# Kernel optimization log

Measured on AMD Instinct MI355X. Metric: run time of the kernel, lower is better.

## Reference

```python
import jax, jax.numpy as jnp
import numpy as np

INPUT_DIM = 1024
OUTPUT_DIM = 1024


def setup_inputs() -> dict:
    key = jax.random.key(0)
    k1, k2, k3, k4 = jax.random.split(key, 4)
    B, S, D = 4, 2048, INPUT_DIM
    src = jax.random.normal(k1, (B, S, D), dtype=jnp.float32)
    tgt = jax.random.normal(k2, (B, S, D), dtype=jnp.float32)
    # nn.Linear(input_dim*2, output_dim): weight [out, in], bias [out]
    bound = 1.0 / np.sqrt(2 * D)
    W = jax.random.uniform(k3, (OUTPUT_DIM, 2 * D), jnp.float32, -bound, bound)
    b = jax.random.uniform(k4, (OUTPUT_DIM,), jnp.float32, -bound, bound)
    return {"src": src, "tgt": tgt, "W": W, "b": b}


def reference(src, tgt, W, b):
    # weight = bmm(tgt, src^T): [B, S_tgt, S_src]
    weight = jnp.einsum("btd,bsd->bts", tgt, src)
    # NOTE: original uses Softmax(dim=1) -> normalizes over the tgt axis
    weight = jax.nn.softmax(weight, axis=1)
    # weighted sum over src positions: [B, S_tgt, D]
    weight_sum = jnp.einsum("bts,bsd->btd", weight, src)
    output = jnp.concatenate([weight_sum, tgt], axis=2)  # [B, S_tgt, 2D]
    output = output @ W.T + b  # [B, S_tgt, output_dim]
    return (output, weight)
```

## Files before the change

### kernel.cpp

```cpp
#include <hip/hip_runtime.h>
#include <stdint.h>


#define B_   4
#define S_   2048
#define D_   1024
#define OUTD 1024

typedef unsigned short ushort_t;
typedef _Float16 half8 __attribute__((ext_vector_type(8)));
typedef float    f32x4 __attribute__((ext_vector_type(4)));

__device__ __forceinline__ ushort_t f2h(float f) {
    union { _Float16 h; ushort_t u; } v;
    v.h = (_Float16)f;
    return v.u;
}
__device__ __forceinline__ float h2f(ushort_t u) {
    union { _Float16 h; ushort_t u; } v;
    v.u = u;
    return (float)v.h;
}

__device__ __forceinline__ void ld16(const ushort_t* g, ushort_t* l) {
    __builtin_amdgcn_global_load_lds(
        (const __attribute__((address_space(1))) void*)g,
        (__attribute__((address_space(3))) void*)l, 16, 0, 0);
}


__global__ void k_split(const float4* __restrict__ src, const float4* __restrict__ tgt,
                        ushort4* __restrict__ sh,
                        ushort4* __restrict__ th, ushort4* __restrict__ tl)
{
    const int64_t n4 = (int64_t)B_ * S_ * D_ / 4;
    for (int64_t i = (int64_t)blockIdx.x * blockDim.x + threadIdx.x; i < n4;
         i += (int64_t)gridDim.x * blockDim.x) {
        float4 s = src[i];
        sh[i] = (ushort4){f2h(s.x), f2h(s.y), f2h(s.z), f2h(s.w)};
        float4 tv = tgt[i];
        ushort4 ht = {f2h(tv.x), f2h(tv.y), f2h(tv.z), f2h(tv.w)};
        th[i] = ht;
        tl[i] = (ushort4){f2h(tv.x - h2f(ht.x)), f2h(tv.y - h2f(ht.y)),
                          f2h(tv.z - h2f(ht.z)), f2h(tv.w - h2f(ht.w))};
    }
}

__global__ void k_wconv(const float4* __restrict__ W, ushort4* __restrict__ wb)
{
    const int64_t n4 = (int64_t)OUTD * 2 * D_ / 4;
    for (int64_t i = (int64_t)blockIdx.x * blockDim.x + threadIdx.x; i < n4;
         i += (int64_t)gridDim.x * blockDim.x) {
        float4 w = W[i];
        wb[i] = (ushort4){f2h(w.x), f2h(w.y), f2h(w.z), f2h(w.w)};
    }
}

__launch_bounds__(256)
__global__ void k_gemm_logits(const ushort_t* __restrict__ Ah, const ushort_t* __restrict__ Al,
                              const ushort_t* __restrict__ Bs,
                              float* __restrict__ C,
                              float* __restrict__ pm, float* __restrict__ ps)
{
    const int M = S_, N = S_, K = D_;
    int b = blockIdx.z;
    Ah += (int64_t)b * M * K;  Al += (int64_t)b * M * K;
    Bs += (int64_t)b * N * K;
    C  += (int64_t)b * M * N;

    __shared__ __align__(16) ushort_t sAh[128 * 32], sAl[128 * 32], sB[128 * 32];
    __shared__ float red_m[2][128], red_s[2][128];

    int t    = threadIdx.x;
    int m0   = blockIdx.y * 128, n0 = blockIdx.x * 128;
    int wave = t >> 6, lane = t & 63;
    int wr   = (wave >> 1) * 64, wc = (wave & 1) * 64;
    int l15  = lane & 15, quad = lane >> 4;

    f32x4 acc[4][4];
#pragma unroll
    for (int i = 0; i < 4; i++)
#pragma unroll
        for (int j = 0; j < 4; j++) acc[i][j] = (f32x4){0.f, 0.f, 0.f, 0.f};

    int srow = t >> 2;
    int scol = (t & 3) * 8;

    const ushort_t* gAh0 = Ah + (int64_t)(m0 + srow) * K + scol;
    const ushort_t* gAh1 = gAh0 + (int64_t)64 * K;
    const ushort_t* gAl0 = Al + (int64_t)(m0 + srow) * K + scol;
    const ushort_t* gAl1 = gAl0 + (int64_t)64 * K;
    const ushort_t* gB0  = Bs + (int64_t)(n0 + srow) * K + scol;
    const ushort_t* gB1  = gB0 + (int64_t)64 * K;

    ushort_t* lAh0 = sAh + wave * 512;  ushort_t* lAh1 = sAh + 2048 + wave * 512;
    ushort_t* lAl0 = sAl + wave * 512;  ushort_t* lAl1 = sAl + 2048 + wave * 512;
    ushort_t* lB0  = sB  + wave * 512;  ushort_t* lB1  = sB  + 2048 + wave * 512;

    for (int k0 = 0; k0 < K; k0 += 32) {
        ld16(gAh0, lAh0);  ld16(gAh1, lAh1);
        ld16(gAl0, lAl0);  ld16(gAl1, lAl1);
        ld16(gB0,  lB0);   ld16(gB1,  lB1);
        gAh0 += 32; gAh1 += 32; gAl0 += 32; gAl1 += 32; gB0 += 32; gB1 += 32;
        __syncthreads();

        half8 ah[4], al[4], bf[4];
#pragma unroll
        for (int i = 0; i < 4; i++) {
            ah[i] = *(const half8*)(&sAh[(wr + i * 16 + l15) * 32 + quad * 8]);
            al[i] = *(const half8*)(&sAl[(wr + i * 16 + l15) * 32 + quad * 8]);
        }
#pragma unroll
        for (int j = 0; j < 4; j++)
            bf[j] = *(const half8*)(&sB[(wc + j * 16 + l15) * 32 + quad * 8]);
#pragma unroll
        for (int i = 0; i < 4; i++)
#pragma unroll
            for (int j = 0; j < 4; j++) {
                acc[i][j] = __builtin_amdgcn_mfma_f32_16x16x32_f16(ah[i], bf[j], acc[i][j], 0, 0, 0);
                acc[i][j] = __builtin_amdgcn_mfma_f32_16x16x32_f16(al[i], bf[j], acc[i][j], 0, 0, 0);
            }
        __syncthreads();
    }

#pragma unroll
    for (int i = 0; i < 4; i++) {
        int row_base = m0 + wr + i * 16 + quad * 4;
#pragma unroll
        for (int j = 0; j < 4; j++) {
            int col = n0 + wc + j * 16 + l15;
#pragma unroll
            for (int r = 0; r < 4; r++)
                C[(int64_t)(row_base + r) * N + col] = acc[i][j][r];
        }
    }

    int rowhalf = wave >> 1;
#pragma unroll
    for (int j = 0; j < 4; j++) {
        float m = -3.0e38f;
#pragma unroll
        for (int i = 0; i < 4; i++)
#pragma unroll
            for (int r = 0; r < 4; r++) m = fmaxf(m, acc[i][j][r]);
        float s = 0.f;
#pragma unroll
        for (int i = 0; i < 4; i++)
#pragma unroll
            for (int r = 0; r < 4; r++) s += __expf(acc[i][j][r] - m);
#pragma unroll
        for (int d = 16; d <= 32; d <<= 1) {
            float m2 = __shfl_xor(m, d, 64);
            float s2 = __shfl_xor(s, d, 64);
            float nm = fmaxf(m, m2);
            s = s * __expf(m - nm) + s2 * __expf(m2 - nm);
            m = nm;
        }
        if (lane < 16) {
            red_m[rowhalf][wc + j * 16 + l15] = m;
            red_s[rowhalf][wc + j * 16 + l15] = s;
        }
    }
    __syncthreads();
    if (t < 128) {
        float ma = red_m[0][t], mb = red_m[1][t];
        float sa = red_s[0][t], sb = red_s[1][t];
        float m = fmaxf(ma, mb);
        float s = sa * __expf(ma - m) + sb * __expf(mb - m);
        int idx = blockIdx.y * (B_ * S_) + b * S_ + n0 + t;
        pm[idx] = m;
        ps[idx] = s;
    }
}


__global__ void k_colstats2(const float* __restrict__ pm, const float* __restrict__ ps,
                            float* __restrict__ cmax, float* __restrict__ cinv)
{
    int i = blockIdx.x * 256 + threadIdx.x;
    float m = -3.0e38f;
#pragma unroll
    for (int c = 0; c < 16; c++) m = fmaxf(m, pm[c * (B_ * S_) + i]);
    float sum = 0.f;
#pragma unroll
    for (int c = 0; c < 16; c++) sum += ps[c * (B_ * S_) + i] * __expf(pm[c * (B_ * S_) + i] - m);
    cmax[i] = m;
    cinv[i] = 1.0f / sum;
}

__global__ void k_softmax_norm(float4* __restrict__ L, const float4* __restrict__ cmax4,
                               const float4* __restrict__ cinv4, ushort4* __restrict__ wbf)
{
    const int64_t n4 = (int64_t)B_ * S_ * S_ / 4;
    for (int64_t i = (int64_t)blockIdx.x * blockDim.x + threadIdx.x; i < n4;
         i += (int64_t)gridDim.x * blockDim.x) {
        int b  = (int)(i >> 20);
        int c4 = (int)(i & 511);
        float4 x  = L[i];
        float4 cm = cmax4[b * 512 + c4];
        float4 ci = cinv4[b * 512 + c4];
        float4 w;
        w.x = __expf(x.x - cm.x) * ci.x;
        w.y = __expf(x.y - cm.y) * ci.y;
        w.z = __expf(x.z - cm.z) * ci.z;
        w.w = __expf(x.w - cm.w) * ci.w;
        L[i] = w;
        wbf[i] = (ushort4){f2h(w.x), f2h(w.y), f2h(w.z), f2h(w.w)};
    }
}

__launch_bounds__(256)
__global__ void k_gemm_nt_f16(const ushort_t* __restrict__ A, int lda, int64_t bsA,
                              const ushort_t* __restrict__ Bm, int ldb, int64_t bsB,
                              ushort_t* __restrict__ C, int ldc, int64_t bsC, int K)
{
    int b = blockIdx.z;
    A  += (int64_t)b * bsA;
    Bm += (int64_t)b * bsB;
    C  += (int64_t)b * bsC;

    __shared__ __align__(16) ushort_t sA[128 * 64], sB[128 * 64];

    int t    = threadIdx.x;
    int m0   = blockIdx.y * 128, n0 = blockIdx.x * 128;
    int wave = t >> 6, lane = t & 63;
    int wr   = (wave >> 1) * 64, wc = (wave & 1) * 64;
    int l15  = lane & 15, quad = lane >> 4;
    int e7   = l15 & 7;

    f32x4 acc[4][4];
#pragma unroll
    for (int i = 0; i < 4; i++)
#pragma unroll
        for (int j = 0; j < 4; j++) acc[i][j] = (f32x4){0.f, 0.f, 0.f, 0.f};

    int srow = t >> 3;
    int scol = (((t & 7) ^ (srow & 7)) * 8);

    const ushort_t* gA = A  + (int64_t)(m0 + srow) * lda + scol;
    const ushort_t* gB = Bm + (int64_t)(n0 + srow) * ldb + scol;
    ushort_t* lA = sA + wave * 512;
    ushort_t* lB = sB + wave * 512;

    for (int k0 = 0; k0 < K; k0 += 64) {
#pragma unroll
        for (int j = 0; j < 4; j++) {
            ld16(gA + (int64_t)(j * 32) * lda + k0, lA + j * 2048);
            ld16(gB + (int64_t)(j * 32) * ldb + k0, lB + j * 2048);
        }
        __syncthreads();
#pragma unroll
        for (int ks = 0; ks < 64; ks += 32) {
            int gchunk = (ks >> 3) + quad;
            int slot   = (gchunk ^ e7) * 8;
            half8 af[4], bf[4];
#pragma unroll
            for (int i = 0; i < 4; i++)
                af[i] = *(const half8*)(&sA[(wr + i * 16 + l15) * 64 + slot]);
#pragma unroll
            for (int j = 0; j < 4; j++)
                bf[j] = *(const half8*)(&sB[(wc + j * 16 + l15) * 64 + slot]);
#pragma unroll
            for (int i = 0; i < 4; i++)
#pragma unroll
                for (int j = 0; j < 4; j++)
                    acc[i][j] = __builtin_amdgcn_mfma_f32_16x16x32_f16(af[i], bf[j], acc[i][j], 0, 0, 0);
        }
        __syncthreads();
    }

#pragma unroll
    for (int i = 0; i < 4; i++) {
        int row_base = m0 + wr + i * 16 + quad * 4;
#pragma unroll
        for (int j = 0; j < 4; j++) {
            int col = n0 + wc + j * 16 + l15;
#pragma unroll
            for (int r = 0; r < 4; r++)
                C[(int64_t)(row_base + r) * ldc + col] = f2h(acc[i][j][r]);
        }
    }
}

__launch_bounds__(256)
__global__ void k_gemm_final(const ushort_t* __restrict__ Wt, const ushort_t* __restrict__ PT,
                             const ushort_t* __restrict__ Q, const float* __restrict__ bias,
                             float* __restrict__ out)
{
    const int K = S_, N = OUTD;
    int b = blockIdx.z;
    const ushort_t* A  = Wt + (int64_t)b * S_ * S_;
    const ushort_t* Bm = PT + (int64_t)b * OUTD * S_;
    const ushort_t* Qb = Q  + (int64_t)b * S_ * OUTD;
    float* Cb = out + (int64_t)b * S_ * OUTD;

    __shared__ __align__(16) ushort_t sA[128 * 64], sB[128 * 64];

    int t    = threadIdx.x;
    int m0   = blockIdx.y * 128, n0 = blockIdx.x * 128;
    int wave = t >> 6, lane = t & 63;
    int wr   = (wave >> 1) * 64, wc = (wave & 1) * 64;
    int l15  = lane & 15, quad = lane >> 4;
    int e7   = l15 & 7;

    f32x4 acc[4][4];
#pragma unroll
    for (int i = 0; i < 4; i++)
#pragma unroll
        for (int j = 0; j < 4; j++) acc[i][j] = (f32x4){0.f, 0.f, 0.f, 0.f};

    int srow = t >> 3;
    int scol = (((t & 7) ^ (srow & 7)) * 8);

    const ushort_t* gA = A  + (int64_t)(m0 + srow) * K + scol;
    const ushort_t* gB = Bm + (int64_t)(n0 + srow) * K + scol;
    ushort_t* lA = sA + wave * 512;
    ushort_t* lB = sB + wave * 512;

    for (int k0 = 0; k0 < K; k0 += 64) {
#pragma unroll
        for (int j = 0; j < 4; j++) {
            ld16(gA + (int64_t)(j * 32) * K + k0, lA + j * 2048);
            ld16(gB + (int64_t)(j * 32) * K + k0, lB + j * 2048);
        }
        __syncthreads();
#pragma unroll
        for (int ks = 0; ks < 64; ks += 32) {
            int gchunk = (ks >> 3) + quad;
            int slot   = (gchunk ^ e7) * 8;
            half8 af[4], bf[4];
#pragma unroll
            for (int i = 0; i < 4; i++)
                af[i] = *(const half8*)(&sA[(wr + i * 16 + l15) * 64 + slot]);
#pragma unroll
            for (int j = 0; j < 4; j++)
                bf[j] = *(const half8*)(&sB[(wc + j * 16 + l15) * 64 + slot]);
#pragma unroll
            for (int i = 0; i < 4; i++)
#pragma unroll
                for (int j = 0; j < 4; j++)
                    acc[i][j] = __builtin_amdgcn_mfma_f32_16x16x32_f16(af[i], bf[j], acc[i][j], 0, 0, 0);
        }
        __syncthreads();
    }

#pragma unroll
    for (int i = 0; i < 4; i++) {
        int row_base = m0 + wr + i * 16 + quad * 4;
#pragma unroll
        for (int j = 0; j < 4; j++) {
            int col = n0 + wc + j * 16 + l15;
            float bv = bias[col];
#pragma unroll
            for (int r = 0; r < 4; r++) {
                int64_t idx = (int64_t)(row_base + r) * N + col;
                Cb[idx] = acc[i][j][r] + h2f(Qb[idx]) + bv;
            }
        }
    }
}


extern "C" void kernel_launch(void* const* d_in, const int* in_sizes, int n_in,
                              void* d_out, int out_size, void* d_ws, size_t ws_size,
                              hipStream_t stream)
{
    const float* src  = (const float*)d_in[0];
    const float* tgt  = (const float*)d_in[1];
    const float* W    = (const float*)d_in[2];
    const float* bias = (const float*)d_in[3];

    float* out = (float*)d_out;
    float* Lw  = out + (size_t)B_ * S_ * OUTD;

    char*  ws = (char*)d_ws;
    size_t o  = 0;
    auto take = [&](size_t bytes) -> char* {
        char* p = ws + o;
        o += (bytes + 255) & ~(size_t)255;
        return p;
    };
    const size_t ELEMS = (size_t)B_ * S_ * D_;
    ushort_t* sh   = (ushort_t*)take(ELEMS * 2);
    ushort_t* th   = (ushort_t*)take(ELEMS * 2);
    ushort_t* tl   = (ushort_t*)take(ELEMS * 2);
    ushort_t* wbf  = (ushort_t*)take((size_t)B_ * S_ * S_ * 2);
    ushort_t* wb   = (ushort_t*)take((size_t)OUTD * 2 * D_ * 2);
    ushort_t* PT   = (ushort_t*)take((size_t)B_ * OUTD * S_ * 2);
    ushort_t* Qb   = (ushort_t*)take((size_t)B_ * S_ * OUTD * 2);
    float*    pm   = (float*)take(16 * (size_t)B_ * S_ * 4);
    float*    ps   = (float*)take(16 * (size_t)B_ * S_ * 4);
    float*    cmax = (float*)take((size_t)B_ * S_ * 4);
    float*    cinv = (float*)take((size_t)B_ * S_ * 4);
    (void)ws_size; (void)in_sizes; (void)n_in; (void)out_size;

    k_split<<<dim3(2048), dim3(256), 0, stream>>>((const float4*)src, (const float4*)tgt,
                                                  (ushort4*)sh, (ushort4*)th, (ushort4*)tl);
    k_wconv<<<dim3(512), dim3(256), 0, stream>>>((const float4*)W, (ushort4*)wb);

    k_gemm_nt_f16<<<dim3(16, 8, 4), dim3(256), 0, stream>>>(
        wb, 2 * D_, 0,
        sh, D_, (int64_t)S_ * D_,
        PT, S_, (int64_t)OUTD * S_, D_);

    k_gemm_nt_f16<<<dim3(8, 16, 4), dim3(256), 0, stream>>>(
        th, D_, (int64_t)S_ * D_,
        wb + D_, 2 * D_, 0,
        Qb, OUTD, (int64_t)S_ * OUTD, D_);

    k_gemm_logits<<<dim3(16, 16, 4), dim3(256), 0, stream>>>(th, tl, sh, Lw, pm, ps);

    k_colstats2<<<dim3(32), dim3(256), 0, stream>>>(pm, ps, cmax, cinv);
    k_softmax_norm<<<dim3(2048), dim3(256), 0, stream>>>((float4*)Lw, (const float4*)cmax,
                                                         (const float4*)cinv, (ushort4*)wbf);

    k_gemm_final<<<dim3(8, 16, 4), dim3(256), 0, stream>>>(wbf, PT, Qb, bias, out);
}
```

Before: 371.8 us.

## Enlarge logits GEMM tile to 256x256 with double-buffered swizzled LDS

The logits GEMM now uses 512-thread blocks computing 256x256 tiles, with a 2-stage LDS ping-pong so the next K-slice loads are issued before the current slice's MFMAs. The LDS layout is XOR-swizzled to avoid bank conflicts, and s_setprio raises priority around the MFMA groups. The grid shrinks to 8x8x4 and the column-stats pass now reduces 8 partials instead of 16. This aims to improve data reuse and hide global latency, but raises registers per thread (128 accumulators) and LDS use, which may reduce occupancy or cause spills.

```diff
diff --git a/kernel.cpp b/kernel.cpp
--- a/kernel.cpp
+++ b/kernel.cpp
@@ -56,7 +56,7 @@
     }
 }
 
-__launch_bounds__(256)
+__launch_bounds__(512, 2)
 __global__ void k_gemm_logits(const ushort_t* __restrict__ Ah, const ushort_t* __restrict__ Al,
                               const ushort_t* __restrict__ Bs,
                               float* __restrict__ C,
@@ -68,66 +68,115 @@
     Bs += (int64_t)b * N * K;
     C  += (int64_t)b * M * N;
 
-    __shared__ __align__(16) ushort_t sAh[128 * 32], sAl[128 * 32], sB[128 * 32];
-    __shared__ float red_m[2][128], red_s[2][128];
+    __shared__ __align__(16) ushort_t lds[2 * 24576];
+    __shared__ float red_m[4][256], red_s[4][256];
 
     int t    = threadIdx.x;
-    int m0   = blockIdx.y * 128, n0 = blockIdx.x * 128;
+    int m0   = blockIdx.y * 256, n0 = blockIdx.x * 256;
     int wave = t >> 6, lane = t & 63;
-    int wr   = (wave >> 1) * 64, wc = (wave & 1) * 64;
+    int wr   = (wave >> 1) * 64;
+    int wc   = (wave & 1) * 128;
     int l15  = lane & 15, quad = lane >> 4;
 
-    f32x4 acc[4][4];
+    f32x4 acc[4][8];
 #pragma unroll
     for (int i = 0; i < 4; i++)
 #pragma unroll
-        for (int j = 0; j < 4; j++) acc[i][j] = (f32x4){0.f, 0.f, 0.f, 0.f};
-
-    int srow = t >> 2;
-    int scol = (t & 3) * 8;
-
-    const ushort_t* gAh0 = Ah + (int64_t)(m0 + srow) * K + scol;
-    const ushort_t* gAh1 = gAh0 + (int64_t)64 * K;
-    const ushort_t* gAl0 = Al + (int64_t)(m0 + srow) * K + scol;
-    const ushort_t* gAl1 = gAl0 + (int64_t)64 * K;
-    const ushort_t* gB0  = Bs + (int64_t)(n0 + srow) * K + scol;
-    const ushort_t* gB1  = gB0 + (int64_t)64 * K;
-
-    ushort_t* lAh0 = sAh + wave * 512;  ushort_t* lAh1 = sAh + 2048 + wave * 512;
-    ushort_t* lAl0 = sAl + wave * 512;  ushort_t* lAl1 = sAl + 2048 + wave * 512;
-    ushort_t* lB0  = sB  + wave * 512;  ushort_t* lB1  = sB  + 2048 + wave * 512;
-
-    for (int k0 = 0; k0 < K; k0 += 32) {
-        ld16(gAh0, lAh0);  ld16(gAh1, lAh1);
-        ld16(gAl0, lAl0);  ld16(gAl1, lAl1);
-        ld16(gB0,  lB0);   ld16(gB1,  lB1);
-        gAh0 += 32; gAh1 += 32; gAl0 += 32; gAl1 += 32; gB0 += 32; gB1 += 32;
-        __syncthreads();
-
+        for (int j = 0; j < 8; j++) acc[i][j] = (f32x4){0.f, 0.f, 0.f, 0.f};
+
+    int pr   = t >> 3;
+    int slot = t & 7;
+    int cg   = slot ^ (pr & 7);
+    int srow = pr * 2 + (cg >> 2);
+    int scol = (cg & 3) * 8;
+
+    const ushort_t* gAh = Ah + (int64_t)(m0 + srow) * K + scol;
+    const ushort_t* gAl = Al + (int64_t)(m0 + srow) * K + scol;
+    const ushort_t* gB  = Bs + (int64_t)(n0 + srow) * K + scol;
+    const int64_t rstep = (int64_t)128 * K;
+
+    auto stage = [&](int bufi, int kofs) {
+        ushort_t* Lb = lds + bufi * 24576 + t * 8;
+        ld16(gAh + kofs,         Lb);
+        ld16(gAh + rstep + kofs, Lb + 4096);
+        ld16(gAl + kofs,         Lb + 8192);
+        ld16(gAl + rstep + kofs, Lb + 12288);
+        ld16(gB  + kofs,         Lb + 16384);
+        ld16(gB  + rstep + kofs, Lb + 20480);
+    };
+
+    int aoff[4], boff[8];
+#pragma unroll
+    for (int i = 0; i < 4; i++) {
+        int R = wr + i * 16 + l15;
+        int p = R >> 1, c = ((R & 1) << 2) + quad;
+        aoff[i] = p * 64 + ((c ^ (p & 7)) << 3);
+    }
+#pragma unroll
+    for (int j = 0; j < 8; j++) {
+        int R = wc + j * 16 + l15;
+        int p = R >> 1, c = ((R & 1) << 2) + quad;
+        boff[j] = p * 64 + ((c ^ (p & 7)) << 3);
+    }
+
+    stage(0, 0);
+    int buf = 0;
+
+    for (int kt = 0; kt < 32; ++kt) {
+        asm volatile("s_waitcnt vmcnt(0)" ::: "memory");
+        __builtin_amdgcn_s_barrier();
+        asm volatile("" ::: "memory");
+        __builtin_amdgcn_sched_barrier(0);
+
+        if (kt < 31) stage(buf ^ 1, (kt + 1) * 32);
+
+        const ushort_t* Lb = lds + buf * 24576;
         half8 ah[4], al[4], bf[4];
 #pragma unroll
         for (int i = 0; i < 4; i++) {
-            ah[i] = *(const half8*)(&sAh[(wr + i * 16 + l15) * 32 + quad * 8]);
-            al[i] = *(const half8*)(&sAl[(wr + i * 16 + l15) * 32 + quad * 8]);
-        }
-#pragma unroll
-        for (int j = 0; j < 4; j++)
-            bf[j] = *(const half8*)(&sB[(wc + j * 16 + l15) * 32 + quad * 8]);
-#pragma unroll
-        for (int i = 0; i < 4; i++)
-#pragma unroll
-            for (int j = 0; j < 4; j++) {
+            ah[i] = *(const half8*)(Lb + aoff[i]);
+            al[i] = *(const half8*)(Lb + 8192 + aoff[i]);
+        }
+#pragma unroll
+        for (int j = 0; j < 4; j++) bf[j] = *(const half8*)(Lb + 16384 + boff[j]);
+
+        __builtin_amdgcn_s_setprio(1);
+#pragma unroll
+        for (int i = 0; i < 4; i++)
+#pragma unroll
+            for (int j = 0; j < 4; j++)
                 acc[i][j] = __builtin_amdgcn_mfma_f32_16x16x32_f16(ah[i], bf[j], acc[i][j], 0, 0, 0);
+#pragma unroll
+        for (int i = 0; i < 4; i++)
+#pragma unroll
+            for (int j = 0; j < 4; j++)
                 acc[i][j] = __builtin_amdgcn_mfma_f32_16x16x32_f16(al[i], bf[j], acc[i][j], 0, 0, 0);
-            }
-        __syncthreads();
+        __builtin_amdgcn_s_setprio(0);
+
+#pragma unroll
+        for (int j = 0; j < 4; j++) bf[j] = *(const half8*)(Lb + 16384 + boff[4 + j]);
+
+        __builtin_amdgcn_s_setprio(1);
+#pragma unroll
+        for (int i = 0; i < 4; i++)
+#pragma unroll
+            for (int j = 0; j < 4; j++)
+                acc[i][4 + j] = __builtin_amdgcn_mfma_f32_16x16x32_f16(ah[i], bf[j], acc[i][4 + j], 0, 0, 0);
+#pragma unroll
+        for (int i = 0; i < 4; i++)
+#pragma unroll
+            for (int j = 0; j < 4; j++)
+                acc[i][4 + j] = __builtin_amdgcn_mfma_f32_16x16x32_f16(al[i], bf[j], acc[i][4 + j], 0, 0, 0);
+        __builtin_amdgcn_s_setprio(0);
+
+        buf ^= 1;
     }
 
 #pragma unroll
     for (int i = 0; i < 4; i++) {
         int row_base = m0 + wr + i * 16 + quad * 4;
 #pragma unroll
-        for (int j = 0; j < 4; j++) {
+        for (int j = 0; j < 8; j++) {
             int col = n0 + wc + j * 16 + l15;
 #pragma unroll
             for (int r = 0; r < 4; r++)
@@ -135,9 +184,9 @@
         }
     }
 
-    int rowhalf = wave >> 1;
-#pragma unroll
-    for (int j = 0; j < 4; j++) {
+    int wrow = wave >> 1;
+#pragma unroll
+    for (int j = 0; j < 8; j++) {
         float m = -3.0e38f;
 #pragma unroll
         for (int i = 0; i < 4; i++)
@@ -157,16 +206,18 @@
             m = nm;
         }
         if (lane < 16) {
-            red_m[rowhalf][wc + j * 16 + l15] = m;
-            red_s[rowhalf][wc + j * 16 + l15] = s;
+            red_m[wrow][wc + j * 16 + l15] = m;
+            red_s[wrow][wc + j * 16 + l15] = s;
         }
     }
     __syncthreads();
-    if (t < 128) {
-        float ma = red_m[0][t], mb = red_m[1][t];
-        float sa = red_s[0][t], sb = red_s[1][t];
-        float m = fmaxf(ma, mb);
-        float s = sa * __expf(ma - m) + sb * __expf(mb - m);
+    if (t < 256) {
+        float m = red_m[0][t];
+#pragma unroll
+        for (int w = 1; w < 4; w++) m = fmaxf(m, red_m[w][t]);
+        float s = 0.f;
+#pragma unroll
+        for (int w = 0; w < 4; w++) s += red_s[w][t] * __expf(red_m[w][t] - m);
         int idx = blockIdx.y * (B_ * S_) + b * S_ + n0 + t;
         pm[idx] = m;
         ps[idx] = s;
@@ -180,10 +231,10 @@
     int i = blockIdx.x * 256 + threadIdx.x;
     float m = -3.0e38f;
 #pragma unroll
-    for (int c = 0; c < 16; c++) m = fmaxf(m, pm[c * (B_ * S_) + i]);
+    for (int c = 0; c < 8; c++) m = fmaxf(m, pm[c * (B_ * S_) + i]);
     float sum = 0.f;
 #pragma unroll
-    for (int c = 0; c < 16; c++) sum += ps[c * (B_ * S_) + i] * __expf(pm[c * (B_ * S_) + i] - m);
+    for (int c = 0; c < 8; c++) sum += ps[c * (B_ * S_) + i] * __expf(pm[c * (B_ * S_) + i] - m);
     cmax[i] = m;
     cinv[i] = 1.0f / sum;
 }
@@ -408,7 +459,7 @@
         wb + D_, 2 * D_, 0,
         Qb, OUTD, (int64_t)S_ * OUTD, D_);
 
-    k_gemm_logits<<<dim3(16, 16, 4), dim3(256), 0, stream>>>(th, tl, sh, Lw, pm, ps);
+    k_gemm_logits<<<dim3(8, 8, 4), dim3(512), 0, stream>>>(th, tl, sh, Lw, pm, ps);
 
     k_colstats2<<<dim3(32), dim3(256), 0, stream>>>(pm, ps, cmax, cinv);
     k_softmax_norm<<<dim3(2048), dim3(256), 0, stream>>>((float4*)Lw, (const float4*)cmax,
```

New measurement: 358.5 us. -3.6%, faster.
